# Performance work log

Measured on AMD Instinct MI355X. Metric: run time of the kernel, lower is better.

The kernel has to match this reference:

```python
import jax, jax.numpy as jnp
import numpy as np

N, E, B = 50000, 400000, 50
F_IN, HID, HEADS, F_OUT = 128, 32, 8, 64
HC = HID * HEADS  # 256


def gat_conv(x, src, dst, W, a_s, a_d, b, n):
    """PyG-style GATConv (concat=True, negative_slope=0.2), inference mode."""
    H, C = a_s.shape
    h = (x @ W).reshape(n, H, C)                       # [N,H,C]
    alpha_s = (h * a_s).sum(-1)                        # [N,H]
    alpha_d = (h * a_d).sum(-1)                        # [N,H]
    logits = jax.nn.leaky_relu(alpha_s[src] + alpha_d[dst], 0.2)  # [E,H]
    m = jax.ops.segment_max(logits, dst, num_segments=n)
    m = jnp.where(jnp.isfinite(m), m, 0.0)
    e = jnp.exp(logits - m[dst])
    den = jax.ops.segment_sum(e, dst, num_segments=n)
    alpha = e / (den[dst] + 1e-16)                     # segment softmax over dst
    out = jax.ops.segment_sum(h[src] * alpha[:, :, None], dst, num_segments=n)
    return out.reshape(n, H * C) + b


def setup_inputs() -> dict:
    key = jax.random.key(0)
    ks = jax.random.split(key, 24)
    s = 0.1
    inp = {
        "x": jax.random.normal(ks[0], (N, F_IN), jnp.float32),
        "edge_index": jax.random.randint(ks[1], (2, E), 0, N),
        "batch": jnp.sort(jax.random.randint(ks[2], (N,), 0, B)),
        "W1": jax.random.normal(ks[3], (F_IN, HC), jnp.float32) * s,
        "a_src1": jax.random.normal(ks[4], (HEADS, HID), jnp.float32) * s,
        "a_dst1": jax.random.normal(ks[5], (HEADS, HID), jnp.float32) * s,
        "b1": jnp.zeros((HC,), jnp.float32),
        "W2": jax.random.normal(ks[6], (HC, HC), jnp.float32) * s,
        "a_src2": jax.random.normal(ks[7], (1, HC), jnp.float32) * s,
        "a_dst2": jax.random.normal(ks[8], (1, HC), jnp.float32) * s,
        "b2": jnp.zeros((HC,), jnp.float32),
        "W3": jax.random.normal(ks[9], (HC, HC), jnp.float32) * s,
        "a_src3": jax.random.normal(ks[10], (1, HC), jnp.float32) * s,
        "a_dst3": jax.random.normal(ks[11], (1, HC), jnp.float32) * s,
        "b3": jnp.zeros((HC,), jnp.float32),
        "W4": jax.random.normal(ks[12], (HC, F_OUT), jnp.float32) * s,
        "a_src4": jax.random.normal(ks[13], (1, F_OUT), jnp.float32) * s,
        "a_dst4": jax.random.normal(ks[14], (1, F_OUT), jnp.float32) * s,
        "b4": jnp.zeros((F_OUT,), jnp.float32),
        "Wl": jax.random.normal(ks[15], (F_OUT, 1), jnp.float32) * s,
        "bl": jnp.zeros((1,), jnp.float32),
    }
    return inp


def reference(x, edge_index, batch, W1, a_src1, a_dst1, b1, W2, a_src2, a_dst2, b2,
              W3, a_src3, a_dst3, b3, W4, a_src4, a_dst4, b4, Wl, bl):
    n = x.shape[0]
    loop = jnp.arange(n)
    src = jnp.concatenate([edge_index[0], loop])  # add self loops (PyG default)
    dst = jnp.concatenate([edge_index[1], loop])
    x = jax.nn.elu(gat_conv(x, src, dst, W1, a_src1, a_dst1, b1, n))
    x = jax.nn.elu(gat_conv(x, src, dst, W2, a_src2, a_dst2, b2, n))
    x = jax.nn.elu(gat_conv(x, src, dst, W3, a_src3, a_dst3, b3, n))
    x_gat = gat_conv(x, src, dst, W4, a_src4, a_dst4, b4, n)
    # to_dense_batch(x_gat, batch).mean(dim=1): sum per graph / max graph size
    counts = jax.ops.segment_sum(jnp.ones((n,), x_gat.dtype), batch, num_segments=B)
    max_nodes = counts.max()
    pooled = jax.ops.segment_sum(x_gat, batch, num_segments=B) / max_nodes  # [B,F_OUT]
    return pooled @ Wl + bl  # [B,1]
```

## Files before the change

kernel.cpp:

```cpp
#include <hip/hip_runtime.h>
#include <math.h>


typedef __attribute__((ext_vector_type(8))) short short8;
typedef __attribute__((ext_vector_type(4))) float f32x4;

__device__ __forceinline__ unsigned short f2bf(float f) {
  unsigned int u = __builtin_bit_cast(unsigned int, f);
  unsigned int r = u + 0x7FFFu + ((u >> 16) & 1u);
  return (unsigned short)(r >> 16);
}
__device__ __forceinline__ float bf2f(unsigned short h) {
  unsigned int u = ((unsigned int)h) << 16;
  return __builtin_bit_cast(float, u);
}
__device__ __forceinline__ unsigned short f2h(float f) {
  _Float16 h = (_Float16)f;
  return __builtin_bit_cast(unsigned short, h);
}
__device__ __forceinline__ float h2f(unsigned short u) {
  return (float)__builtin_bit_cast(_Float16, u);
}

__device__ __forceinline__ void gload16(const unsigned short* g, unsigned short* l) {
  __builtin_amdgcn_global_load_lds(
      (const __attribute__((address_space(1))) void*)g,
      (__attribute__((address_space(3))) void*)l, 16, 0, 0);
}

template<int H>
__global__ __launch_bounds__(256) void k_gemm_mfma(
    const unsigned short* __restrict__ A2, const unsigned short* __restrict__ Wt,
    unsigned short* __restrict__ C, const float* __restrict__ avec_s,
    const float* __restrict__ avec_d, float* __restrict__ outS,
    float* __restrict__ outD, int M, int Kb, int Nc)
{
  __shared__ unsigned short lds[16384];
  unsigned short* As = lds;
  unsigned short* Bs = lds + 8192;
  const int tid = threadIdx.x;
  const int w = tid >> 6, l = tid & 63;
  const int row0 = blockIdx.x * 128, col0 = blockIdx.y * 128;
  const int wr = w >> 1, wc = w & 1;
  const int fr = l & 15, kg = l >> 4;
  const int xr = (fr & 7) << 4;
  const int sK = 2 * Kb;
  const int csrc = 8 * ((l & 7) ^ ((l >> 3) & 7));
  const int rstage = w * 32 + (l >> 3);

  f32x4 acc[4][4];
  #pragma unroll
  for (int i = 0; i < 4; i++)
    #pragma unroll
    for (int j = 0; j < 4; j++) acc[i][j] = (f32x4){0.f, 0.f, 0.f, 0.f};

  for (int kp = 0; kp < sK; kp += 64) {
    #pragma unroll
    for (int i = 0; i < 4; i++) {
      int r = rstage + i * 8;
      gload16(&A2[(size_t)(row0 + r) * sK + (kp + csrc)], &As[w * 2048 + i * 512]);
      gload16(&Wt[(size_t)(col0 + r) * sK + (kp + csrc)], &Bs[w * 2048 + i * 512]);
    }
    __syncthreads();
    #pragma unroll
    for (int kk = 0; kk < 2; kk++) {
      short8 a[4], b[4];
      #pragma unroll
      for (int mi = 0; mi < 4; mi++) {
        int r = wr * 64 + mi * 16 + fr;
        int off = r * 128 + ((kk * 64 + kg * 16) ^ xr);
        a[mi] = *(const short8*)((const char*)As + off);
      }
      #pragma unroll
      for (int ni = 0; ni < 4; ni++) {
        int c = wc * 64 + ni * 16 + fr;
        int off = c * 128 + ((kk * 64 + kg * 16) ^ xr);
        b[ni] = *(const short8*)((const char*)Bs + off);
      }
      #pragma unroll
      for (int mi = 0; mi < 4; mi++)
        #pragma unroll
        for (int ni = 0; ni < 4; ni++)
          acc[mi][ni] = __builtin_amdgcn_mfma_f32_16x16x32_bf16(
              a[mi], b[ni], acc[mi][ni], 0, 0, 0);
    }
    __syncthreads();
  }

  #pragma unroll
  for (int mi = 0; mi < 4; mi++)
    #pragma unroll
    for (int ni = 0; ni < 4; ni++)
      #pragma unroll
      for (int rr = 0; rr < 4; rr++) {
        int row = wr * 64 + mi * 16 + kg * 4 + rr;
        int c = wc * 64 + ni * 16 + fr;
        int sc = c ^ (((row >> 1) & 7) << 3);
        lds[row * 128 + sc] = f2h(acc[mi][ni][rr]);
      }
  __syncthreads();

  constexpr int RW = (H == 8) ? 4 : 16;
  const int Ch = Nc / H;
  const int rbase = tid >> 4;
  const int cc = tid & 15;
  const int c0 = cc * 8;
  const int gc0 = col0 + c0;
  float as8[8], ad8[8];
  #pragma unroll
  for (int j = 0; j < 8; j++) {
    bool ok = (gc0 + j) < Nc;
    as8[j] = ok ? avec_s[gc0 + j] : 0.f;
    ad8[j] = ok ? avec_d[gc0 + j] : 0.f;
  }
  #pragma unroll
  for (int i = 0; i < 8; i++) {
    int row = rbase + i * 16;
    int gr = row0 + row;
    int scc = c0 ^ (((row >> 1) & 7) << 3);
    short8 cv = *(const short8*)&lds[row * 128 + scc];
    if (gr < M && gc0 < Nc)
      *(short8*)&C[(size_t)gr * Nc + gc0] = cv;
    float ps = 0.f, pd = 0.f;
    #pragma unroll
    for (int j = 0; j < 8; j++) {
      float cf = h2f((unsigned short)cv[j]);
      ps = fmaf(cf, as8[j], ps);
      pd = fmaf(cf, ad8[j], pd);
    }
    #pragma unroll
    for (int off = 1; off < RW; off <<= 1) {
      ps += __shfl_xor(ps, off);
      pd += __shfl_xor(pd, off);
    }
    if ((tid & (RW - 1)) == 0 && gr < M) {
      int head = gc0 / Ch;
      atomicAdd(&outS[gr * H + head], ps);
      atomicAdd(&outD[gr * H + head], pd);
    }
  }
}

__global__ __launch_bounds__(256) void k_packX(const float* __restrict__ x,
    unsigned short* __restrict__ A2, int N, int Mpad)
{
  int row = blockIdx.x * 8 + (threadIdx.x >> 5);
  int c = (threadIdx.x & 31) * 4;
  if (row >= Mpad) return;
  float4 v = make_float4(0.f, 0.f, 0.f, 0.f);
  if (row < N) v = *(const float4*)&x[(size_t)row * 128 + c];
  float f[4] = {v.x, v.y, v.z, v.w};
  unsigned short hi[4], lo[4];
  #pragma unroll
  for (int i = 0; i < 4; i++) {
    hi[i] = f2bf(f[i]);
    lo[i] = f2bf(f[i] - bf2f(hi[i]));
  }
  size_t base = (size_t)row * 256 + c;
  *(uint2*)&A2[base] = make_uint2((unsigned)hi[0] | ((unsigned)hi[1] << 16),
                                  (unsigned)hi[2] | ((unsigned)hi[3] << 16));
  *(uint2*)&A2[base + 128] = make_uint2((unsigned)lo[0] | ((unsigned)lo[1] << 16),
                                        (unsigned)lo[2] | ((unsigned)lo[3] << 16));
}

__global__ void k_packW(const float* __restrict__ W, unsigned short* __restrict__ Wt,
                        int K, int NC, int NCPAD)
{
  int idx = blockIdx.x * 256 + threadIdx.x;
  int K2 = 2 * K;
  if (idx >= NCPAD * K2) return;
  int c = idx / K2, kp = idx % K2;
  unsigned short o = 0;
  if (c < NC) o = f2bf(W[(size_t)(kp % K) * NC + c]);
  Wt[(size_t)c * K2 + kp] = o;
}

template<int H, int HC, int ELU, int SPLIT>
__global__ __launch_bounds__(256) void k_aggregate(const unsigned short* __restrict__ h,
    const float* __restrict__ as, const float* __restrict__ ad,
    const int* __restrict__ rowptr, const int* __restrict__ col,
    const float* __restrict__ bias, float* __restrict__ xout,
    unsigned short* __restrict__ a2out, int N)
{
  constexpr int VEC = HC / 64;
  constexpr int C = HC / H;
  constexpr int CH = (H == 8) ? 8 : 64;
  __shared__ float wlds[4][64];
  int wave = threadIdx.x >> 6, lane = threadIdx.x & 63;
  int row = blockIdx.x * 4 + wave;
  if (row >= N) return;
  const int cb = lane * VEC;
  const int hdg = cb / C;
  int s0 = rowptr[row], s1 = rowptr[row + 1];

  float adv = (H == 8) ? ad[row * 8 + (lane & 7)] : ad[row];
  float den = 0.f;
  float acc[VEC];
  #pragma unroll
  for (int v = 0; v < VEC; v++) acc[v] = 0.f;

  for (int base = s0; base < s1; base += CH) {
    int cnt = min(CH, s1 - base);
    int eo = (H == 8) ? (lane >> 3) : lane;
    bool valid = eo < cnt;
    int s = col[valid ? (base + eo) : (s1 - 1)];
    float lg = ((H == 8) ? as[s * 8 + (lane & 7)] : as[s]) + adv;
    lg = fmaxf(lg, 0.2f * lg);
    float wgt = valid ? __expf(lg) : 0.f;
    float d = wgt;
    if (H == 8) {
      d += __shfl_xor(d, 8); d += __shfl_xor(d, 16); d += __shfl_xor(d, 32);
      wlds[wave][(lane >> 3) * 8 + (lane & 7)] = wgt;
    } else {
      #pragma unroll
      for (int off = 1; off < 64; off <<= 1) d += __shfl_xor(d, off);
    }
    den += d;
    if (H == 8) {
      asm volatile("s_waitcnt lgkmcnt(0)" ::: "memory");
    }
    #pragma unroll 2
    for (int j = 0; j < cnt; j++) {
      int sj = __builtin_amdgcn_readlane(s, (H == 8) ? (j * 8) : j);
      float wj;
      if constexpr (H == 8) {
        wj = wlds[wave][j * 8 + hdg];
      } else {
        wj = __builtin_bit_cast(float,
              __builtin_amdgcn_readlane(__builtin_bit_cast(int, wgt), j));
      }
      if constexpr (VEC == 4) {
        uint2 raw = *(const uint2*)&h[(size_t)sj * HC + cb];
        acc[0] = fmaf(wj, h2f((unsigned short)(raw.x & 0xFFFF)), acc[0]);
        acc[1] = fmaf(wj, h2f((unsigned short)(raw.x >> 16)),    acc[1]);
        acc[2] = fmaf(wj, h2f((unsigned short)(raw.y & 0xFFFF)), acc[2]);
        acc[3] = fmaf(wj, h2f((unsigned short)(raw.y >> 16)),    acc[3]);
      } else {
        acc[0] = fmaf(wj, h2f(h[(size_t)sj * HC + cb]), acc[0]);
      }
    }
  }
  if (H == 8) den = __shfl(den, hdg);
  float inv = 1.f / (den + 1e-16f);
  float o[VEC];
  #pragma unroll
  for (int v = 0; v < VEC; v++) {
    float t = acc[v] * inv + bias[cb + v];
    if (ELU) t = t > 0.f ? t : expm1f(t);
    o[v] = t;
  }
  if constexpr (SPLIT) {
    unsigned short hi[4], lo[4];
    #pragma unroll
    for (int v = 0; v < 4; v++) {
      hi[v] = f2bf(o[v]);
      lo[v] = f2bf(o[v] - bf2f(hi[v]));
    }
    size_t base = (size_t)row * (2 * HC) + cb;
    *(uint2*)&a2out[base] = make_uint2((unsigned)hi[0] | ((unsigned)hi[1] << 16),
                                       (unsigned)hi[2] | ((unsigned)hi[3] << 16));
    *(uint2*)&a2out[base + HC] = make_uint2((unsigned)lo[0] | ((unsigned)lo[1] << 16),
                                            (unsigned)lo[2] | ((unsigned)lo[3] << 16));
  } else if constexpr (VEC == 4) {
    *(float4*)&xout[(size_t)row * HC + cb] = make_float4(o[0], o[1], o[2], o[3]);
  } else {
    xout[(size_t)row * HC + cb] = o[0];
  }
}

__global__ void k_init(int* deg, float* pool, unsigned short* A2, int N, int B,
                       int Mpad) {
  int i = blockIdx.x * 256 + threadIdx.x;
  if (i < N) deg[i] = 1;
  if (i < B * 64) pool[i] = 0.f;
  int padn = (Mpad - N) * 512;
  if (i < padn) A2[(size_t)N * 512 + i] = 0;
}

__global__ void k_deg(const int* __restrict__ ei, int* deg, int E) {
  int e = blockIdx.x * 256 + threadIdx.x;
  if (e < E) atomicAdd(&deg[ei[E + e]], 1);
}

__global__ void k_counts(const int* __restrict__ bat, int* cnt, int N, int B) {
  int b = threadIdx.x;
  if (b >= B) return;
  int lo0 = 0, hi0 = N;
  while (lo0 < hi0) { int mid = (lo0 + hi0) >> 1; if (bat[mid] < b) lo0 = mid + 1; else hi0 = mid; }
  int lo1 = lo0, hi1 = N;
  while (lo1 < hi1) { int mid = (lo1 + hi1) >> 1; if (bat[mid] < b + 1) lo1 = mid + 1; else hi1 = mid; }
  cnt[b] = lo1 - lo0;
}

__global__ __launch_bounds__(256) void k_scan1(const int* __restrict__ deg,
                                               int* csum, int N, int chunk) {
  int bid = blockIdx.x, t = threadIdx.x;
  int lo = bid * chunk, hi = min(lo + chunk, N);
  int s = 0;
  for (int i = lo + t; i < hi; i += 256) s += deg[i];
  #pragma unroll
  for (int off = 32; off; off >>= 1) s += __shfl_xor(s, off);
  __shared__ int sh[4];
  if ((t & 63) == 0) sh[t >> 6] = s;
  __syncthreads();
  if (t == 0) csum[bid] = sh[0] + sh[1] + sh[2] + sh[3];
}

__global__ __launch_bounds__(256) void k_scan2(const int* __restrict__ csum,
                                               int* coff) {
  __shared__ int s[256];
  int t = threadIdx.x;
  int v0 = csum[t];
  s[t] = v0;
  for (int off = 1; off < 256; off <<= 1) {
    __syncthreads();
    int v = (t >= off) ? s[t - off] : 0;
    __syncthreads();
    s[t] += v;
  }
  __syncthreads();
  coff[t] = s[t] - v0;
}

__global__ __launch_bounds__(256) void k_scan3(const int* __restrict__ deg,
    const int* __restrict__ coff, int* rowptr, int* cursor, int N, int chunk) {
  __shared__ int s[256];
  int bid = blockIdx.x, t = threadIdx.x;
  int i = bid * chunk + t;
  int v = (t < chunk && i < N) ? deg[i] : 0;
  s[t] = v;
  for (int off = 1; off < 256; off <<= 1) {
    __syncthreads();
    int x = (t >= off) ? s[t - off] : 0;
    __syncthreads();
    s[t] += x;
  }
  __syncthreads();
  int excl = s[t] - v + coff[bid];
  if (t < chunk && i < N) {
    rowptr[i] = excl;
    cursor[i] = excl;
    if (i == N - 1) rowptr[N] = excl + v;
  }
}

__global__ void k_scatter(const int* __restrict__ ei, int* cursor, int* col,
                          int E, int N) {
  int idx = blockIdx.x * 256 + threadIdx.x;
  if (idx >= E + N) return;
  int s, d;
  if (idx < E) { s = ei[idx]; d = ei[E + idx]; }
  else         { s = d = idx - E; }
  int pos = atomicAdd(&cursor[d], 1);
  col[pos] = s;
}

__global__ __launch_bounds__(256) void k_pool(const float* __restrict__ xg,
    const int* __restrict__ bat, float* pool, int N) {
  int lane = threadIdx.x & 63, w = threadIdx.x >> 6;
  int base = (blockIdx.x * 4 + w) * 16;
  if (base >= N) return;
  int end = min(base + 16, N);
  float local = 0.f;
  int curb = bat[base];
  for (int n = base; n < end; n++) {
    int b = bat[n];
    if (b != curb) {
      atomicAdd(&pool[curb * 64 + lane], local);
      local = 0.f; curb = b;
    }
    local += xg[(size_t)n * 64 + lane];
  }
  atomicAdd(&pool[curb * 64 + lane], local);
}

__global__ void k_final(const float* __restrict__ pool, const int* __restrict__ cnt,
    const float* __restrict__ Wl, const float* __restrict__ bl,
    float* __restrict__ out, int B) {
  int lane = threadIdx.x;
  int c = (lane < B) ? cnt[lane] : 0;
  #pragma unroll
  for (int off = 32; off; off >>= 1) c = max(c, __shfl_xor(c, off));
  float invm = 1.f / (float)c;
  float wl = Wl[lane];
  for (int b = 0; b < B; b++) {
    float ps = pool[b * 64 + lane] * wl;
    #pragma unroll
    for (int off = 32; off; off >>= 1) ps += __shfl_xor(ps, off);
    if (lane == 0) out[b] = ps * invm + bl[0];
  }
}

extern "C" void kernel_launch(void* const* d_in, const int* in_sizes, int n_in,
                              void* d_out, int out_size, void* d_ws, size_t ws_size,
                              hipStream_t stream)
{
  (void)n_in; (void)ws_size;
  const float* x   = (const float*)d_in[0];
  const int*   ei  = (const int*)d_in[1];
  const int*   bat = (const int*)d_in[2];
  const float* W1  = (const float*)d_in[3];
  const float* as1 = (const float*)d_in[4];
  const float* ad1 = (const float*)d_in[5];
  const float* b1  = (const float*)d_in[6];
  const float* W2  = (const float*)d_in[7];
  const float* as2 = (const float*)d_in[8];
  const float* ad2 = (const float*)d_in[9];
  const float* b2  = (const float*)d_in[10];
  const float* W3  = (const float*)d_in[11];
  const float* as3 = (const float*)d_in[12];
  const float* ad3 = (const float*)d_in[13];
  const float* b3  = (const float*)d_in[14];
  const float* W4  = (const float*)d_in[15];
  const float* as4 = (const float*)d_in[16];
  const float* ad4 = (const float*)d_in[17];
  const float* b4  = (const float*)d_in[18];
  const float* Wl  = (const float*)d_in[19];
  const float* bl  = (const float*)d_in[20];
  float* out = (float*)d_out;

  const int N = in_sizes[0] / 128;
  const int E = in_sizes[1] / 2;
  const int B = out_size;
  const int Mpad = ((N + 127) / 128) * 128;

  char* p = (char*)d_ws;
  auto alloc = [&](size_t bytes) -> void* {
    void* r = (void*)p;
    p += ((bytes + 255) & ~(size_t)255);
    return r;
  };
  unsigned short* A2 = (unsigned short*)alloc((size_t)Mpad * 512 * 2);
  unsigned short* hbuf = (unsigned short*)alloc((size_t)N * 256 * 2);
  unsigned short* w2t1 = (unsigned short*)alloc((size_t)256 * 512 * 2);
  unsigned short* w2t2 = (unsigned short*)alloc((size_t)256 * 512 * 2);
  unsigned short* w2t3 = (unsigned short*)alloc((size_t)256 * 512 * 2);
  unsigned short* w2t4 = (unsigned short*)alloc((size_t)128 * 512 * 2);
  float* aAll  = (float*)alloc((size_t)N * 22 * 4);
  float* aSb   = aAll;
  float* aDb   = aAll + (size_t)N * 11;
  int*   deg   = (int*)alloc((size_t)N * 4);
  int*   rowptr= (int*)alloc((size_t)(N + 1) * 4);
  int*   cursor= (int*)alloc((size_t)N * 4);
  int*   col   = (int*)alloc((size_t)(E + N) * 4);
  int*   csum  = (int*)alloc(256 * 4);
  int*   coff  = (int*)alloc(256 * 4);
  float* pool  = (float*)alloc((size_t)B * 64 * 4);
  int*   cnt   = (int*)alloc((size_t)B * 4);
  float* xpool = (float*)A2;

  const int chunk = (N + 255) / 256;
  dim3 T(256);

  k_init<<<dim3((N + 255) / 256), T, 0, stream>>>(deg, pool, A2, N, B, Mpad);
  k_deg<<<dim3((E + 255) / 256), T, 0, stream>>>(ei, deg, E);
  k_counts<<<dim3(1), dim3(64), 0, stream>>>(bat, cnt, N, B);
  k_scan1<<<dim3(256), T, 0, stream>>>(deg, csum, N, chunk);
  k_scan2<<<dim3(1), T, 0, stream>>>(csum, coff);
  k_scan3<<<dim3(256), T, 0, stream>>>(deg, coff, rowptr, cursor, N, chunk);
  k_scatter<<<dim3((E + N + 255) / 256), T, 0, stream>>>(ei, cursor, col, E, N);
  hipMemsetAsync(aAll, 0, (size_t)N * 22 * 4, stream);

  k_packX<<<dim3(Mpad / 8), T, 0, stream>>>(x, A2, N, Mpad);
  k_packW<<<dim3((256 * 256 + 255) / 256), T, 0, stream>>>(W1, w2t1, 128, 256, 256);
  k_packW<<<dim3((256 * 512 + 255) / 256), T, 0, stream>>>(W2, w2t2, 256, 256, 256);
  k_packW<<<dim3((256 * 512 + 255) / 256), T, 0, stream>>>(W3, w2t3, 256, 256, 256);
  k_packW<<<dim3((128 * 512 + 255) / 256), T, 0, stream>>>(W4, w2t4, 256, 64, 128);

  dim3 nwav((N + 3) / 4);
  dim3 g2(Mpad / 128, 2), g1(Mpad / 128, 1);

  float* aS1 = aSb;                 float* aD1 = aDb;
  float* aS2 = aSb + (size_t)N * 8; float* aD2 = aDb + (size_t)N * 8;
  float* aS3 = aSb + (size_t)N * 9; float* aD3 = aDb + (size_t)N * 9;
  float* aS4 = aSb + (size_t)N * 10;float* aD4 = aDb + (size_t)N * 10;

  k_gemm_mfma<8><<<g2, T, 0, stream>>>(A2, w2t1, hbuf, as1, ad1, aS1, aD1, N, 128, 256);
  k_aggregate<8, 256, 1, 1><<<nwav, T, 0, stream>>>(hbuf, aS1, aD1, rowptr, col, b1,
                                                    nullptr, A2, N);
  k_gemm_mfma<1><<<g2, T, 0, stream>>>(A2, w2t2, hbuf, as2, ad2, aS2, aD2, N, 256, 256);
  k_aggregate<1, 256, 1, 1><<<nwav, T, 0, stream>>>(hbuf, aS2, aD2, rowptr, col, b2,
                                                    nullptr, A2, N);
  k_gemm_mfma<1><<<g2, T, 0, stream>>>(A2, w2t3, hbuf, as3, ad3, aS3, aD3, N, 256, 256);
  k_aggregate<1, 256, 1, 1><<<nwav, T, 0, stream>>>(hbuf, aS3, aD3, rowptr, col, b3,
                                                    nullptr, A2, N);
  k_gemm_mfma<1><<<g1, T, 0, stream>>>(A2, w2t4, hbuf, as4, ad4, aS4, aD4, N, 256, 64);
  k_aggregate<1, 64, 0, 0><<<nwav, T, 0, stream>>>(hbuf, aS4, aD4, rowptr, col, b4,
                                                   xpool, nullptr, N);

  k_pool<<<dim3((N + 63) / 64), T, 0, stream>>>(xpool, bat, pool, N);
  k_final<<<dim3(1), dim3(64), 0, stream>>>(pool, cnt, Wl, bl, out, B);
}
```

Measured before the change: 450.5 us.

## Precompute per-edge attention weights and shrink GEMM row tile to 64

Adds a per-edge kernel that computes the leaky-ReLU exponentiated attention weights into a buffer, using a new destination-id array filled by the scatter. The aggregate kernel then reads these weights instead of gathering source/destination scores and computing exp inline. Separately, the MFMA GEMM tile goes from 128x128 to 64x128 rows per block, doubling the grid size to improve occupancy and wave count. The cost is extra kernel launches, an additional per-edge weight buffer written and read each layer, and less data reuse per GEMM block.

```diff
diff --git a/kernel.cpp b/kernel.cpp
--- a/kernel.cpp
+++ b/kernel.cpp
@@ -35,39 +35,43 @@
     const float* __restrict__ avec_d, float* __restrict__ outS,
     float* __restrict__ outD, int M, int Kb, int Nc)
 {
-  __shared__ unsigned short lds[16384];
+  __shared__ unsigned short lds[12288];
   unsigned short* As = lds;
-  unsigned short* Bs = lds + 8192;
+  unsigned short* Bs = lds + 4096;
   const int tid = threadIdx.x;
   const int w = tid >> 6, l = tid & 63;
-  const int row0 = blockIdx.x * 128, col0 = blockIdx.y * 128;
+  const int row0 = blockIdx.x * 64, col0 = blockIdx.y * 128;
   const int wr = w >> 1, wc = w & 1;
   const int fr = l & 15, kg = l >> 4;
   const int xr = (fr & 7) << 4;
   const int sK = 2 * Kb;
   const int csrc = 8 * ((l & 7) ^ ((l >> 3) & 7));
-  const int rstage = w * 32 + (l >> 3);
-
-  f32x4 acc[4][4];
-  #pragma unroll
-  for (int i = 0; i < 4; i++)
+  const int lrow = l >> 3;
+
+  f32x4 acc[2][4];
+  #pragma unroll
+  for (int i = 0; i < 2; i++)
     #pragma unroll
     for (int j = 0; j < 4; j++) acc[i][j] = (f32x4){0.f, 0.f, 0.f, 0.f};
 
   for (int kp = 0; kp < sK; kp += 64) {
     #pragma unroll
+    for (int i = 0; i < 2; i++) {
+      int q = w * 2 + i;
+      gload16(&A2[(size_t)(row0 + q * 8 + lrow) * sK + (kp + csrc)], &As[q * 512]);
+    }
+    #pragma unroll
     for (int i = 0; i < 4; i++) {
-      int r = rstage + i * 8;
-      gload16(&A2[(size_t)(row0 + r) * sK + (kp + csrc)], &As[w * 2048 + i * 512]);
-      gload16(&Wt[(size_t)(col0 + r) * sK + (kp + csrc)], &Bs[w * 2048 + i * 512]);
+      int q = w * 4 + i;
+      gload16(&Wt[(size_t)(col0 + q * 8 + lrow) * sK + (kp + csrc)], &Bs[q * 512]);
     }
     __syncthreads();
     #pragma unroll
     for (int kk = 0; kk < 2; kk++) {
-      short8 a[4], b[4];
+      short8 a[2], b[4];
       #pragma unroll
-      for (int mi = 0; mi < 4; mi++) {
-        int r = wr * 64 + mi * 16 + fr;
+      for (int mi = 0; mi < 2; mi++) {
+        int r = wr * 32 + mi * 16 + fr;
         int off = r * 128 + ((kk * 64 + kg * 16) ^ xr);
         a[mi] = *(const short8*)((const char*)As + off);
       }
@@ -78,7 +82,7 @@
         b[ni] = *(const short8*)((const char*)Bs + off);
       }
       #pragma unroll
-      for (int mi = 0; mi < 4; mi++)
+      for (int mi = 0; mi < 2; mi++)
         #pragma unroll
         for (int ni = 0; ni < 4; ni++)
           acc[mi][ni] = __builtin_amdgcn_mfma_f32_16x16x32_bf16(
@@ -88,12 +92,12 @@
   }
 
   #pragma unroll
-  for (int mi = 0; mi < 4; mi++)
+  for (int mi = 0; mi < 2; mi++)
     #pragma unroll
     for (int ni = 0; ni < 4; ni++)
       #pragma unroll
       for (int rr = 0; rr < 4; rr++) {
-        int row = wr * 64 + mi * 16 + kg * 4 + rr;
+        int row = wr * 32 + mi * 16 + kg * 4 + rr;
         int c = wc * 64 + ni * 16 + fr;
         int sc = c ^ (((row >> 1) & 7) << 3);
         lds[row * 128 + sc] = f2h(acc[mi][ni][rr]);
@@ -114,7 +118,7 @@
     ad8[j] = ok ? avec_d[gc0 + j] : 0.f;
   }
   #pragma unroll
-  for (int i = 0; i < 8; i++) {
+  for (int i = 0; i < 4; i++) {
     int row = rbase + i * 16;
     int gr = row0 + row;
     int scc = c0 ^ (((row >> 1) & 7) << 3);
@@ -175,9 +179,23 @@
   Wt[(size_t)c * K2 + kp] = o;
 }
 
+template<int H>
+__global__ void k_wcomp(const float* __restrict__ aS, const float* __restrict__ aD,
+    const int* __restrict__ col, const int* __restrict__ rid,
+    float* __restrict__ wbuf, int M)
+{
+  int idx = blockIdx.x * 256 + threadIdx.x;
+  if (idx >= M) return;
+  int e = idx / H, hd = idx % H;
+  int s = col[e], r = rid[e];
+  float lg = aS[s * H + hd] + aD[r * H + hd];
+  lg = fmaxf(lg, 0.2f * lg);
+  wbuf[idx] = __expf(lg);
+}
+
 template<int H, int HC, int ELU, int SPLIT>
 __global__ __launch_bounds__(256) void k_aggregate(const unsigned short* __restrict__ h,
-    const float* __restrict__ as, const float* __restrict__ ad,
+    const float* __restrict__ wbuf,
     const int* __restrict__ rowptr, const int* __restrict__ col,
     const float* __restrict__ bias, float* __restrict__ xout,
     unsigned short* __restrict__ a2out, int N)
@@ -193,7 +211,6 @@
   const int hdg = cb / C;
   int s0 = rowptr[row], s1 = rowptr[row + 1];
 
-  float adv = (H == 8) ? ad[row * 8 + (lane & 7)] : ad[row];
   float den = 0.f;
   float acc[VEC];
   #pragma unroll
@@ -204,13 +221,11 @@
     int eo = (H == 8) ? (lane >> 3) : lane;
     bool valid = eo < cnt;
     int s = col[valid ? (base + eo) : (s1 - 1)];
-    float lg = ((H == 8) ? as[s * 8 + (lane & 7)] : as[s]) + adv;
-    lg = fmaxf(lg, 0.2f * lg);
-    float wgt = valid ? __expf(lg) : 0.f;
-    float d = wgt;
-    if (H == 8) {
+    float wv = valid ? wbuf[(size_t)base * H + lane] : 0.f;
+    float d = wv;
+    if constexpr (H == 8) {
       d += __shfl_xor(d, 8); d += __shfl_xor(d, 16); d += __shfl_xor(d, 32);
-      wlds[wave][(lane >> 3) * 8 + (lane & 7)] = wgt;
+      wlds[wave][lane] = wv;
     } else {
       #pragma unroll
       for (int off = 1; off < 64; off <<= 1) d += __shfl_xor(d, off);
@@ -227,7 +242,7 @@
         wj = wlds[wave][j * 8 + hdg];
       } else {
         wj = __builtin_bit_cast(float,
-              __builtin_amdgcn_readlane(__builtin_bit_cast(int, wgt), j));
+              __builtin_amdgcn_readlane(__builtin_bit_cast(int, wv), j));
       }
       if constexpr (VEC == 4) {
         uint2 raw = *(const uint2*)&h[(size_t)sj * HC + cb];
@@ -256,11 +271,11 @@
       hi[v] = f2bf(o[v]);
       lo[v] = f2bf(o[v] - bf2f(hi[v]));
     }
-    size_t base = (size_t)row * (2 * HC) + cb;
-    *(uint2*)&a2out[base] = make_uint2((unsigned)hi[0] | ((unsigned)hi[1] << 16),
-                                       (unsigned)hi[2] | ((unsigned)hi[3] << 16));
-    *(uint2*)&a2out[base + HC] = make_uint2((unsigned)lo[0] | ((unsigned)lo[1] << 16),
-                                            (unsigned)lo[2] | ((unsigned)lo[3] << 16));
+    size_t b2 = (size_t)row * (2 * HC) + cb;
+    *(uint2*)&a2out[b2] = make_uint2((unsigned)hi[0] | ((unsigned)hi[1] << 16),
+                                     (unsigned)hi[2] | ((unsigned)hi[3] << 16));
+    *(uint2*)&a2out[b2 + HC] = make_uint2((unsigned)lo[0] | ((unsigned)lo[1] << 16),
+                                          (unsigned)lo[2] | ((unsigned)lo[3] << 16));
   } else if constexpr (VEC == 4) {
     *(float4*)&xout[(size_t)row * HC + cb] = make_float4(o[0], o[1], o[2], o[3]);
   } else {
@@ -345,7 +360,7 @@
 }
 
 __global__ void k_scatter(const int* __restrict__ ei, int* cursor, int* col,
-                          int E, int N) {
+                          int* rid, int E, int N) {
   int idx = blockIdx.x * 256 + threadIdx.x;
   if (idx >= E + N) return;
   int s, d;
@@ -353,6 +368,7 @@
   else         { s = d = idx - E; }
   int pos = atomicAdd(&cursor[d], 1);
   col[pos] = s;
+  rid[pos] = d;
 }
 
 __global__ __launch_bounds__(256) void k_pool(const float* __restrict__ xg,
@@ -423,6 +439,7 @@
   const int E = in_sizes[1] / 2;
   const int B = out_size;
   const int Mpad = ((N + 127) / 128) * 128;
+  const int EN = E + N;
 
   char* p = (char*)d_ws;
   auto alloc = [&](size_t bytes) -> void* {
@@ -439,10 +456,12 @@
   float* aAll  = (float*)alloc((size_t)N * 22 * 4);
   float* aSb   = aAll;
   float* aDb   = aAll + (size_t)N * 11;
+  float* wbuf  = (float*)alloc((size_t)EN * 8 * 4);
   int*   deg   = (int*)alloc((size_t)N * 4);
   int*   rowptr= (int*)alloc((size_t)(N + 1) * 4);
   int*   cursor= (int*)alloc((size_t)N * 4);
-  int*   col   = (int*)alloc((size_t)(E + N) * 4);
+  int*   col   = (int*)alloc((size_t)EN * 4);
+  int*   rid   = (int*)alloc((size_t)EN * 4);
   int*   csum  = (int*)alloc(256 * 4);
   int*   coff  = (int*)alloc(256 * 4);
   float* pool  = (float*)alloc((size_t)B * 64 * 4);
@@ -458,7 +477,7 @@
   k_scan1<<<dim3(256), T, 0, stream>>>(deg, csum, N, chunk);
   k_scan2<<<dim3(1), T, 0, stream>>>(csum, coff);
   k_scan3<<<dim3(256), T, 0, stream>>>(deg, coff, rowptr, cursor, N, chunk);
-  k_scatter<<<dim3((E + N + 255) / 256), T, 0, stream>>>(ei, cursor, col, E, N);
+  k_scatter<<<dim3((EN + 255) / 256), T, 0, stream>>>(ei, cursor, col, rid, E, N);
   hipMemsetAsync(aAll, 0, (size_t)N * 22 * 4, stream);
 
   k_packX<<<dim3(Mpad / 8), T, 0, stream>>>(x, A2, N, Mpad);
@@ -468,7 +487,8 @@
   k_packW<<<dim3((128 * 512 + 255) / 256), T, 0, stream>>>(W4, w2t4, 256, 64, 128);
 
   dim3 nwav((N + 3) / 4);
-  dim3 g2(Mpad / 128, 2), g1(Mpad / 128, 1);
+  dim3 g2(Mpad / 64, 2), g1(Mpad / 64, 1);
+  dim3 gw8((EN * 8 + 255) / 256), gw1((EN + 255) / 256);
 
   float* aS1 = aSb;                 float* aD1 = aDb;
   float* aS2 = aSb + (size_t)N * 8; float* aD2 = aDb + (size_t)N * 8;
@@ -476,16 +496,20 @@
   float* aS4 = aSb + (size_t)N * 10;float* aD4 = aDb + (size_t)N * 10;
 
   k_gemm_mfma<8><<<g2, T, 0, stream>>>(A2, w2t1, hbuf, as1, ad1, aS1, aD1, N, 128, 256);
-  k_aggregate<8, 256, 1, 1><<<nwav, T, 0, stream>>>(hbuf, aS1, aD1, rowptr, col, b1,
+  k_wcomp<8><<<gw8, T, 0, stream>>>(aS1, aD1, col, rid, wbuf, EN * 8);
+  k_aggregate<8, 256, 1, 1><<<nwav, T, 0, stream>>>(hbuf, wbuf, rowptr, col, b1,
                                                     nullptr, A2, N);
   k_gemm_mfma<1><<<g2, T, 0, stream>>>(A2, w2t2, hbuf, as2, ad2, aS2, aD2, N, 256, 256);
-  k_aggregate<1, 256, 1, 1><<<nwav, T, 0, stream>>>(hbuf, aS2, aD2, rowptr, col, b2,
+  k_wcomp<1><<<gw1, T, 0, stream>>>(aS2, aD2, col, rid, wbuf, EN);
+  k_aggregate<1, 256, 1, 1><<<nwav, T, 0, stream>>>(hbuf, wbuf, rowptr, col, b2,
                                                     nullptr, A2, N);
   k_gemm_mfma<1><<<g2, T, 0, stream>>>(A2, w2t3, hbuf, as3, ad3, aS3, aD3, N, 256, 256);
-  k_aggregate<1, 256, 1, 1><<<nwav, T, 0, stream>>>(hbuf, aS3, aD3, rowptr, col, b3,
+  k_wcomp<1><<<gw1, T, 0, stream>>>(aS3, aD3, col, rid, wbuf, EN);
+  k_aggregate<1, 256, 1, 1><<<nwav, T, 0, stream>>>(hbuf, wbuf, rowptr, col, b3,
                                                     nullptr, A2, N);
   k_gemm_mfma<1><<<g1, T, 0, stream>>>(A2, w2t4, hbuf, as4, ad4, aS4, aD4, N, 256, 64);
-  k_aggregate<1, 64, 0, 0><<<nwav, T, 0, stream>>>(hbuf, aS4, aD4, rowptr, col, b4,
+  k_wcomp<1><<<gw1, T, 0, stream>>>(aS4, aD4, col, rid, wbuf, EN);
+  k_aggregate<1, 64, 0, 0><<<nwav, T, 0, stream>>>(hbuf, wbuf, rowptr, col, b4,
                                                    xpool, nullptr, N);
 
   k_pool<<<dim3((N + 63) / 64), T, 0, stream>>>(xpool, bat, pool, N);
```

New measurement: 462.9 us. 1.03x slower.
